# Kernel tuning notes

Measured on AMD Instinct MI355X. Metric: run time of the kernel, lower is better.

The kernel has to match this reference:

```python
import jax, jax.numpy as jnp
import numpy as np

B, V, T, C, HIN, WIN = 1, 6, 3, 256, 32, 32
NH = 8
LN_EPS = 1e-5


def setup_inputs() -> dict:
    key = jax.random.key(0)
    ks = jax.random.split(key, 14)
    s = 0.02
    lim = 1.0 / np.sqrt(C)
    def lin_w(k):
        return jax.random.uniform(k, (C, C), jnp.float32, -lim, lim)
    return {
        "history_feats": jax.random.normal(ks[0], (B, V, T, C, HIN, WIN), jnp.float32),
        "query_embed": jax.random.normal(ks[1], (1, C, 1, 1), jnp.float32) * s,
        "camera_pos_embed": jax.random.normal(ks[2], (V, C), jnp.float32) * s,
        "temporal_pos_embed": jax.random.normal(ks[3], (T, C), jnp.float32) * s,
        "spatial_pos_embed": jax.random.normal(ks[4], (1, C, 1, 1), jnp.float32) * s,
        "q_w": lin_w(ks[5]), "q_b": jnp.zeros((C,), jnp.float32),
        "k_w": lin_w(ks[6]), "k_b": jnp.zeros((C,), jnp.float32),
        "v_w": lin_w(ks[7]), "v_b": jnp.zeros((C,), jnp.float32),
        "o_w": lin_w(ks[8]), "o_b": jnp.zeros((C,), jnp.float32),
        "ln_g": jnp.ones((C,), jnp.float32),
        "ln_b": jnp.zeros((C,), jnp.float32),
        "query_cam_idx": 0,
        "H": 32,
        "W": 32,
    }


def reference(history_feats, query_embed, camera_pos_embed, temporal_pos_embed,
              spatial_pos_embed, q_w, q_b, k_w, k_b, v_w, v_b, o_w, o_b,
              ln_g, ln_b, query_cam_idx, H, W):
    B_, V_, T_, C_, Hin, Win = history_feats.shape
    dh = C_ // NH
    # --- build query: [B, H*W, C] ---
    q = query_embed + camera_pos_embed[query_cam_idx][None, :, None, None] + spatial_pos_embed
    q = jnp.broadcast_to(q, (B_, C_, H, W)).reshape(B_, C_, H * W).transpose(0, 2, 1)
    kv = (history_feats
          + temporal_pos_embed[None, None, :, :, None, None]
          + camera_pos_embed[None, :, None, :, None, None])
    kv = kv.transpose(0, 1, 2, 4, 5, 3).reshape(B_, V_ * T_ * Hin * Win, C_)
    # --- projections (torch Linear: x @ W.T + b) ---
    qp = q @ q_w.T + q_b
    kp = kv @ k_w.T + k_b
    vp = kv @ v_w.T + v_b
    # --- split heads: [B, NH, L, dh] ---
    qh = qp.reshape(B_, H * W, NH, dh).transpose(0, 2, 1, 3)
    kh = kp.reshape(B_, -1, NH, dh).transpose(0, 2, 1, 3)
    vh = vp.reshape(B_, -1, NH, dh).transpose(0, 2, 1, 3)
    scale = float(dh) ** -0.5
    attn = jax.nn.softmax(jnp.einsum('bhqd,bhkd->bhqk', qh, kh) * scale, axis=-1)
    out = jnp.einsum('bhqk,bhkd->bhqd', attn, vh)
    out = out.transpose(0, 2, 1, 3).reshape(B_, H * W, C_)
    out = out @ o_w.T + o_b
    # --- LayerNorm over channel dim ---
    mu = out.mean(-1, keepdims=True)
    var = ((out - mu) ** 2).mean(-1, keepdims=True)
    out = (out - mu) * jax.lax.rsqrt(var + LN_EPS) * ln_g + ln_b
    return out.transpose(0, 2, 1).reshape(B_, C_, H, W)
```

## Files before the change

kernel.cpp:

```cpp
#include <hip/hip_runtime.h>
#include <hip/hip_fp16.h>

typedef const float* fcp;

#define C_    256
#define NH_   8
#define DH_   32
#define VT_   18
#define HWK   1024
#define L_    (VT_*HWK)
#define SCALE_ 0.17677669529663687f

#define EMB_OFF  0
#define WF_OFF   4608
#define BB_OFF   6656
#define PS_OFF   6720
#define Y_OFF    9024
#define Z_OFF    9280
#define CTXP_OFF 9536

__device__ __forceinline__ float blockReduceSum256(float v){
  __shared__ float red[4];
  #pragma unroll
  for (int off = 32; off; off >>= 1) v += __shfl_xor(v, off, 64);
  const int lane = threadIdx.x & 63, w = threadIdx.x >> 6;
  __syncthreads();
  if (lane == 0) red[w] = v;
  __syncthreads();
  return red[0] + red[1] + red[2] + red[3];
}

__global__ void k_fold(fcp qe, fcp cam, fcp tpe, fcp spe, const int* __restrict__ cidx,
                       fcp qw, fcp qb, fcp kw, fcp kb, float* __restrict__ ws){
  __shared__ float qvS[C_];
  __shared__ float qpS[DH_];
  const int b = blockIdx.x, t = threadIdx.x, lane = t & 63, wv = t >> 6;
  const int ci = cidx[0];
  qvS[t] = qe[t] + cam[ci*C_ + t] + spe[t];
  {
    const int v = b/3, tt = b - v*3;
    ws[EMB_OFF + b*C_ + t] = tpe[tt*C_ + t] + cam[v*C_ + t];
  }
  __syncthreads();
  if (b < 8){
    #pragma unroll
    for (int i = 0; i < 8; i++){
      const int r = b*DH_ + wv*8 + i;
      fcp qr = qw + (size_t)r*C_;
      float v = qr[lane]*qvS[lane] + qr[64+lane]*qvS[64+lane]
              + qr[128+lane]*qvS[128+lane] + qr[192+lane]*qvS[192+lane];
      #pragma unroll
      for (int off = 32; off; off >>= 1) v += __shfl_xor(v, off, 64);
      if (lane == 0) qpS[wv*8 + i] = v + qb[r];
    }
    __syncthreads();
    float acc = 0.f;
    #pragma unroll 8
    for (int d = 0; d < DH_; d++)
      acc += qpS[d] * kw[(size_t)(b*DH_ + d)*C_ + t];
    ws[WF_OFF + b*C_ + t] = SCALE_ * acc;
    if (t == 0){
      float bb = 0.f;
      for (int d = 0; d < DH_; d++) bb += qpS[d] * kb[b*DH_ + d];
      ws[BB_OFF + b] = SCALE_ * bb;
    }
  }
}

__global__ void k_attn(fcp feats, float* __restrict__ ws){
  __shared__ __align__(16) float wf[C_*8];
  __shared__ float redS[32];
  __shared__ float basef[8];
  __shared__ __align__(16) float pred[8*512];
  __shared__ float pexS[64*8];
  __shared__ __half fS[8*32*66];
  const int bid = blockIdx.x, vt = bid >> 4, sc = bid & 15, t = threadIdx.x;

  for (int idx = t; idx < 2048; idx += 512){
    const int h = idx >> 8, c = idx & 255;
    wf[c*8 + h] = ws[WF_OFF + idx];
  }
  __syncthreads();
  if (t < 256){
    const float e = ws[EMB_OFF + vt*C_ + t];
    const float4 wa = *(const float4*)&wf[t*8];
    const float4 wb = *(const float4*)&wf[t*8 + 4];
    float pb[8] = {e*wa.x, e*wa.y, e*wa.z, e*wa.w, e*wb.x, e*wb.y, e*wb.z, e*wb.w};
    #pragma unroll
    for (int h = 0; h < 8; h++){
      float v = pb[h];
      #pragma unroll
      for (int off = 32; off; off >>= 1) v += __shfl_xor(v, off, 64);
      if ((t & 63) == 0) redS[(t >> 6)*8 + h] = v;
    }
  }
  __syncthreads();
  if (t < 8) basef[t] = redS[t] + redS[8+t] + redS[16+t] + redS[24+t] + ws[BB_OFF + t];
  __syncthreads();
  const int s = t & 63, cg = t >> 6;
  fcp fp = feats + ((size_t)vt*C_ + cg*32)*HWK + sc*64 + s;
  float acc[8] = {0,0,0,0,0,0,0,0};
  #pragma unroll 8
  for (int i = 0; i < 32; i++){
    const float fv = fp[(size_t)i*HWK];
    fS[(cg*32 + i)*66 + s] = __float2half(fv);
    const float4 wa = *(const float4*)&wf[(cg*32+i)*8];
    const float4 wb = *(const float4*)&wf[(cg*32+i)*8 + 4];
    acc[0] += fv*wa.x; acc[1] += fv*wa.y; acc[2] += fv*wa.z; acc[3] += fv*wa.w;
    acc[4] += fv*wb.x; acc[5] += fv*wb.y; acc[6] += fv*wb.z; acc[7] += fv*wb.w;
  }
  #pragma unroll
  for (int h = 0; h < 8; h++) pred[cg*512 + h*64 + s] = acc[h];
  __syncthreads();
  {
    const int h1 = t >> 6, tok = t & 63;
    float sum = basef[h1];
    #pragma unroll
    for (int cg2 = 0; cg2 < 8; cg2++) sum += pred[cg2*512 + t];
    const float e = __expf(sum);
    pexS[tok*8 + h1] = e;
    float v = e;
    #pragma unroll
    for (int off = 32; off; off >>= 1) v += __shfl_xor(v, off, 64);
    if (tok == 0) ws[PS_OFF + bid*8 + h1] = v;
  }
  __syncthreads();
  const int lane = t & 63, hB = lane & 7, isub = lane >> 3;
  float aB[4] = {0.f, 0.f, 0.f, 0.f};
  #pragma unroll 8
  for (int s2 = 0; s2 < 64; s2++){
    const float pe = pexS[s2*8 + hB];
    #pragma unroll
    for (int p = 0; p < 4; p++)
      aB[p] += pe * __half2float(fS[(cg*32 + p*8 + isub)*66 + s2]);
  }
  float* outp = ws + CTXP_OFF + (size_t)bid*2048;
  #pragma unroll
  for (int p = 0; p < 4; p++)
    outp[hB*256 + cg*32 + p*8 + isub] = aB[p];
}

__global__ void k_vproj(fcp vw, fcp vb, float* __restrict__ ws){
  __shared__ float psS[288*8];
  const int r = blockIdx.x, t = threadIdx.x, h = r >> 5;
  for (int i = t; i < 288*8; i += 256) psS[i] = ws[PS_OFF + i];
  __syncthreads();
  float ctx = 0.f;
  const float* pp = ws + CTXP_OFF + h*256 + t;
  #pragma unroll 8
  for (int b = 0; b < 288; b++) ctx += pp[(size_t)b*2048];
  float denom = 0.f, embP = 0.f;
  for (int vt = 0; vt < VT_; vt++){
    float P = 0.f;
    #pragma unroll
    for (int sc2 = 0; sc2 < 16; sc2++) P += psS[(vt*16 + sc2)*8 + h];
    denom += P;
    embP  += ws[EMB_OFF + vt*C_ + t] * P;
  }
  const float ctxn = (ctx + embP) / denom;
  float v = vw[(size_t)r*C_ + t] * ctxn;
  v = blockReduceSum256(v);
  if (t == 0) ws[Y_OFF + r] = v + vb[r];
}

__global__ void k_oproj(fcp ow, fcp ob, float* __restrict__ ws){
  const int r = blockIdx.x, t = threadIdx.x;
  float v = ow[(size_t)r*C_ + t] * ws[Y_OFF + t];
  v = blockReduceSum256(v);
  if (t == 0) ws[Z_OFF + r] = v + ob[r];
}

__global__ void k_out(fcp lng, fcp lnb, const float* __restrict__ ws,
                      float* __restrict__ out, int hw){
  const int c = blockIdx.x, t = threadIdx.x;
  const float z = ws[Z_OFF + t];
  const float s  = blockReduceSum256(z);
  const float s2 = blockReduceSum256(z*z);
  const float mu = s * (1.f/C_);
  const float var = s2 * (1.f/C_) - mu*mu;
  const float rs = rsqrtf(var + 1e-5f);
  const float fin = (ws[Z_OFF + c] - mu) * rs * lng[c] + lnb[c];
  float4 pk = make_float4(fin, fin, fin, fin);
  ((float4*)(out + (size_t)c*hw))[t] = pk;
}

extern "C" void kernel_launch(void* const* d_in, const int* in_sizes, int n_in,
                              void* d_out, int out_size, void* d_ws, size_t ws_size,
                              hipStream_t stream) {
  fcp feats = (fcp)d_in[0];
  fcp qe    = (fcp)d_in[1];
  fcp cam   = (fcp)d_in[2];
  fcp tpe   = (fcp)d_in[3];
  fcp spe   = (fcp)d_in[4];
  fcp qw    = (fcp)d_in[5];
  fcp qb    = (fcp)d_in[6];
  fcp kw    = (fcp)d_in[7];
  fcp kb    = (fcp)d_in[8];
  fcp vw    = (fcp)d_in[9];
  fcp vb    = (fcp)d_in[10];
  fcp ow    = (fcp)d_in[11];
  fcp ob    = (fcp)d_in[12];
  fcp lng   = (fcp)d_in[13];
  fcp lnb   = (fcp)d_in[14];
  const int* cidx = (const int*)d_in[15];
  float* ws = (float*)d_ws;
  float* out = (float*)d_out;
  const int hw = out_size / C_;

  k_fold  <<<18,  256, 0, stream>>>(qe, cam, tpe, spe, cidx, qw, qb, kw, kb, ws);
  k_attn  <<<288, 512, 0, stream>>>(feats, ws);
  k_vproj <<<256, 256, 0, stream>>>(vw, vb, ws);
  k_oproj <<<256, 256, 0, stream>>>(ow, ob, ws);
  k_out   <<<256, 256, 0, stream>>>(lng, lnb, ws, out, hw);
}
```

Measured before the change: 149.0 us.

## Fuse V/O projection and LayerNorm tail into one kernel with atomic partial sums

Attention blocks now accumulate their per-block softmax denominators and context partials straight into global buffers with atomicAdd, instead of writing 288 partial slices to reduce later. The three tail kernels (V projection, O projection, LayerNorm/broadcast) are merged into one kernel. Each of its 128 blocks redundantly recomputes the whole 256-wide GEMV chain and then writes its slice of the output. The P·V inner loop also reads half2 pairs to halve the shared-memory loads. This removes two kernel launches and the large partial-buffer reduction, at the cost of atomic contention, non-deterministic summation order, and redundant per-block weight reads.

```diff
diff --git a/kernel.cpp b/kernel.cpp
--- a/kernel.cpp
+++ b/kernel.cpp
@@ -14,21 +14,8 @@
 #define EMB_OFF  0
 #define WF_OFF   4608
 #define BB_OFF   6656
-#define PS_OFF   6720
-#define Y_OFF    9024
-#define Z_OFF    9280
-#define CTXP_OFF 9536
-
-__device__ __forceinline__ float blockReduceSum256(float v){
-  __shared__ float red[4];
-  #pragma unroll
-  for (int off = 32; off; off >>= 1) v += __shfl_xor(v, off, 64);
-  const int lane = threadIdx.x & 63, w = threadIdx.x >> 6;
-  __syncthreads();
-  if (lane == 0) red[w] = v;
-  __syncthreads();
-  return red[0] + red[1] + red[2] + red[3];
-}
+#define PSVT_OFF 6720
+#define CTX_OFF  6912
 
 __global__ void k_fold(fcp qe, fcp cam, fcp tpe, fcp spe, const int* __restrict__ cidx,
                        fcp qw, fcp qb, fcp kw, fcp kb, float* __restrict__ ws){
@@ -40,6 +27,11 @@
   {
     const int v = b/3, tt = b - v*3;
     ws[EMB_OFF + b*C_ + t] = tpe[tt*C_ + t] + cam[v*C_ + t];
+  }
+  if (b == 8){
+    #pragma unroll
+    for (int i = 0; i < 8; i++) ws[CTX_OFF + i*256 + t] = 0.f;
+    if (t < 144) ws[PSVT_OFF + t] = 0.f;
   }
   __syncthreads();
   if (b < 8){
@@ -73,7 +65,7 @@
   __shared__ float basef[8];
   __shared__ __align__(16) float pred[8*512];
   __shared__ float pexS[64*8];
-  __shared__ __half fS[8*32*66];
+  __shared__ __align__(16) __half fS[8*32*66];
   const int bid = blockIdx.x, vt = bid >> 4, sc = bid & 15, t = threadIdx.x;
 
   for (int idx = t; idx < 2048; idx += 512){
@@ -122,66 +114,102 @@
     float v = e;
     #pragma unroll
     for (int off = 32; off; off >>= 1) v += __shfl_xor(v, off, 64);
-    if (tok == 0) ws[PS_OFF + bid*8 + h1] = v;
+    if (tok == 0) atomicAdd(&ws[PSVT_OFF + vt*8 + h1], v);
   }
   __syncthreads();
   const int lane = t & 63, hB = lane & 7, isub = lane >> 3;
   float aB[4] = {0.f, 0.f, 0.f, 0.f};
-  #pragma unroll 8
-  for (int s2 = 0; s2 < 64; s2++){
-    const float pe = pexS[s2*8 + hB];
-    #pragma unroll
-    for (int p = 0; p < 4; p++)
-      aB[p] += pe * __half2float(fS[(cg*32 + p*8 + isub)*66 + s2]);
-  }
-  float* outp = ws + CTXP_OFF + (size_t)bid*2048;
+  #pragma unroll 4
+  for (int s2 = 0; s2 < 64; s2 += 2){
+    const float pe0 = pexS[s2*8 + hB];
+    const float pe1 = pexS[s2*8 + 8 + hB];
+    #pragma unroll
+    for (int p = 0; p < 4; p++){
+      const __half2 h2 = *(const __half2*)&fS[(cg*32 + p*8 + isub)*66 + s2];
+      const float2 f2 = __half22float2(h2);
+      aB[p] += pe0 * f2.x + pe1 * f2.y;
+    }
+  }
   #pragma unroll
   for (int p = 0; p < 4; p++)
-    outp[hB*256 + cg*32 + p*8 + isub] = aB[p];
-}
-
-__global__ void k_vproj(fcp vw, fcp vb, float* __restrict__ ws){
-  __shared__ float psS[288*8];
-  const int r = blockIdx.x, t = threadIdx.x, h = r >> 5;
-  for (int i = t; i < 288*8; i += 256) psS[i] = ws[PS_OFF + i];
-  __syncthreads();
-  float ctx = 0.f;
-  const float* pp = ws + CTXP_OFF + h*256 + t;
-  #pragma unroll 8
-  for (int b = 0; b < 288; b++) ctx += pp[(size_t)b*2048];
-  float denom = 0.f, embP = 0.f;
-  for (int vt = 0; vt < VT_; vt++){
-    float P = 0.f;
-    #pragma unroll
-    for (int sc2 = 0; sc2 < 16; sc2++) P += psS[(vt*16 + sc2)*8 + h];
-    denom += P;
-    embP  += ws[EMB_OFF + vt*C_ + t] * P;
-  }
-  const float ctxn = (ctx + embP) / denom;
-  float v = vw[(size_t)r*C_ + t] * ctxn;
-  v = blockReduceSum256(v);
-  if (t == 0) ws[Y_OFF + r] = v + vb[r];
-}
-
-__global__ void k_oproj(fcp ow, fcp ob, float* __restrict__ ws){
-  const int r = blockIdx.x, t = threadIdx.x;
-  float v = ow[(size_t)r*C_ + t] * ws[Y_OFF + t];
-  v = blockReduceSum256(v);
-  if (t == 0) ws[Z_OFF + r] = v + ob[r];
-}
-
-__global__ void k_out(fcp lng, fcp lnb, const float* __restrict__ ws,
-                      float* __restrict__ out, int hw){
-  const int c = blockIdx.x, t = threadIdx.x;
-  const float z = ws[Z_OFF + t];
-  const float s  = blockReduceSum256(z);
-  const float s2 = blockReduceSum256(z*z);
-  const float mu = s * (1.f/C_);
-  const float var = s2 * (1.f/C_) - mu*mu;
-  const float rs = rsqrtf(var + 1e-5f);
-  const float fin = (ws[Z_OFF + c] - mu) * rs * lng[c] + lnb[c];
-  float4 pk = make_float4(fin, fin, fin, fin);
-  ((float4*)(out + (size_t)c*hw))[t] = pk;
+    atomicAdd(&ws[CTX_OFF + hB*256 + cg*32 + p*8 + isub], aB[p]);
+}
+
+__global__ void k_tail(fcp vw, fcp vb, fcp ow, fcp ob, fcp lng, fcp lnb,
+                       fcp wsr, float* __restrict__ out, int hw){
+  __shared__ float PS[144];
+  __shared__ float rdS[8];
+  __shared__ __align__(16) float ctxnS[2048];
+  __shared__ __align__(16) float yS[256];
+  __shared__ float zS[256];
+  __shared__ float redA[8], redB[8], mv[2];
+  const int t = threadIdx.x, w = t >> 6, lane = t & 63;
+  if (t < 144) PS[t] = wsr[PSVT_OFF + t];
+  __syncthreads();
+  if (t < 8){
+    float d = 0.f;
+    #pragma unroll
+    for (int vt = 0; vt < VT_; vt++) d += PS[vt*8 + t];
+    rdS[t] = 1.f / d;
+  }
+  __syncthreads();
+  #pragma unroll
+  for (int hc = t; hc < 2048; hc += 512){
+    const int h = hc >> 8, c = hc & 255;
+    float corr = 0.f;
+    #pragma unroll
+    for (int vt = 0; vt < VT_; vt++) corr += wsr[EMB_OFF + vt*C_ + c] * PS[vt*8 + h];
+    ctxnS[hc] = (wsr[CTX_OFF + hc] + corr) * rdS[h];
+  }
+  __syncthreads();
+  {
+    const float4 cv = *(const float4*)&ctxnS[w*256 + lane*4];
+    #pragma unroll 8
+    for (int i = 0; i < 32; i++){
+      const int k = w*32 + i;
+      const float4 a = *(const float4*)&vw[(size_t)k*C_ + lane*4];
+      float v = a.x*cv.x + a.y*cv.y + a.z*cv.z + a.w*cv.w;
+      #pragma unroll
+      for (int off = 32; off; off >>= 1) v += __shfl_xor(v, off, 64);
+      if (lane == 0) yS[k] = v + vb[k];
+    }
+  }
+  __syncthreads();
+  {
+    const float4 yv = *(const float4*)&yS[lane*4];
+    #pragma unroll 8
+    for (int i = 0; i < 32; i++){
+      const int r = w*32 + i;
+      const float4 a = *(const float4*)&ow[(size_t)r*C_ + lane*4];
+      float v = a.x*yv.x + a.y*yv.y + a.z*yv.z + a.w*yv.w;
+      #pragma unroll
+      for (int off = 32; off; off >>= 1) v += __shfl_xor(v, off, 64);
+      if (lane == 0) zS[r] = v + ob[r];
+    }
+  }
+  __syncthreads();
+  const float zv = (t < 256) ? zS[t] : 0.f;
+  float a1 = zv, a2 = zv*zv;
+  #pragma unroll
+  for (int off = 32; off; off >>= 1){
+    a1 += __shfl_xor(a1, off, 64);
+    a2 += __shfl_xor(a2, off, 64);
+  }
+  if (lane == 0){ redA[w] = a1; redB[w] = a2; }
+  __syncthreads();
+  if (t == 0){
+    float s1 = 0.f, s2 = 0.f;
+    #pragma unroll
+    for (int i = 0; i < 8; i++){ s1 += redA[i]; s2 += redB[i]; }
+    const float mu = s1 * (1.f/C_);
+    const float var = s2 * (1.f/C_) - mu*mu;
+    mv[0] = mu; mv[1] = rsqrtf(var + 1e-5f);
+  }
+  __syncthreads();
+  const int tid = blockIdx.x*512 + t;
+  const int c = tid >> 8, quad = tid & 255;
+  const float fin = (zS[c] - mv[0]) * mv[1] * lng[c] + lnb[c];
+  ((float4*)out)[(size_t)c*(hw >> 2) + quad] = make_float4(fin, fin, fin, fin);
 }
 
 extern "C" void kernel_launch(void* const* d_in, const int* in_sizes, int n_in,
@@ -207,9 +235,7 @@
   float* out = (float*)d_out;
   const int hw = out_size / C_;
 
-  k_fold  <<<18,  256, 0, stream>>>(qe, cam, tpe, spe, cidx, qw, qb, kw, kb, ws);
-  k_attn  <<<288, 512, 0, stream>>>(feats, ws);
-  k_vproj <<<256, 256, 0, stream>>>(vw, vb, ws);
-  k_oproj <<<256, 256, 0, stream>>>(ow, ob, ws);
-  k_out   <<<256, 256, 0, stream>>>(lng, lnb, ws, out, hw);
-}
+  k_fold <<<18,  256, 0, stream>>>(qe, cam, tpe, spe, cidx, qw, qb, kw, kb, ws);
+  k_attn <<<288, 512, 0, stream>>>(feats, ws);
+  k_tail <<<128, 512, 0, stream>>>(vw, vb, ow, ob, lng, lnb, ws, out, hw);
+}
```

Result: slower. 168.5 us (+13.1%).

## Accumulate attention partials with atomics instead of per-block buffers

Applied to the files above, without the earlier changes.

Per-block context partials and exp-sum partials are now accumulated directly into small global buffers with atomicAdd, zeroed in k_fold. This removes the 288x2048 partial buffer write and the per-row 288-way reduction that every k_vproj block repeated. The inner PV loop also reads half2 pairs from shared memory to halve LDS instructions. In exchange there is heavy atomic contention: 288 blocks add into the same 2048 floats, and floating-point summation order becomes nondeterministic.

```diff
diff --git a/kernel.cpp b/kernel.cpp
--- a/kernel.cpp
+++ b/kernel.cpp
@@ -14,10 +14,10 @@
 #define EMB_OFF  0
 #define WF_OFF   4608
 #define BB_OFF   6656
-#define PS_OFF   6720
-#define Y_OFF    9024
-#define Z_OFF    9280
-#define CTXP_OFF 9536
+#define PSVT_OFF 6720
+#define CTX_OFF  6912
+#define Y_OFF    8960
+#define Z_OFF    9216
 
 __device__ __forceinline__ float blockReduceSum256(float v){
   __shared__ float red[4];
@@ -41,6 +41,11 @@
     const int v = b/3, tt = b - v*3;
     ws[EMB_OFF + b*C_ + t] = tpe[tt*C_ + t] + cam[v*C_ + t];
   }
+  if (b == 8){
+    #pragma unroll
+    for (int i = 0; i < 8; i++) ws[CTX_OFF + i*256 + t] = 0.f;
+    if (t < 144) ws[PSVT_OFF + t] = 0.f;
+  }
   __syncthreads();
   if (b < 8){
     #pragma unroll
@@ -73,7 +78,7 @@
   __shared__ float basef[8];
   __shared__ __align__(16) float pred[8*512];
   __shared__ float pexS[64*8];
-  __shared__ __half fS[8*32*66];
+  __shared__ __align__(16) __half fS[8*32*66];
   const int bid = blockIdx.x, vt = bid >> 4, sc = bid & 15, t = threadIdx.x;
 
   for (int idx = t; idx < 2048; idx += 512){
@@ -122,41 +127,40 @@
     float v = e;
     #pragma unroll
     for (int off = 32; off; off >>= 1) v += __shfl_xor(v, off, 64);
-    if (tok == 0) ws[PS_OFF + bid*8 + h1] = v;
+    if (tok == 0) atomicAdd(&ws[PSVT_OFF + vt*8 + h1], v);
   }
   __syncthreads();
   const int lane = t & 63, hB = lane & 7, isub = lane >> 3;
   float aB[4] = {0.f, 0.f, 0.f, 0.f};
-  #pragma unroll 8
-  for (int s2 = 0; s2 < 64; s2++){
-    const float pe = pexS[s2*8 + hB];
-    #pragma unroll
-    for (int p = 0; p < 4; p++)
-      aB[p] += pe * __half2float(fS[(cg*32 + p*8 + isub)*66 + s2]);
-  }
-  float* outp = ws + CTXP_OFF + (size_t)bid*2048;
+  #pragma unroll 4
+  for (int s2 = 0; s2 < 64; s2 += 2){
+    const float pe0 = pexS[s2*8 + hB];
+    const float pe1 = pexS[s2*8 + 8 + hB];
+    #pragma unroll
+    for (int p = 0; p < 4; p++){
+      const __half2 h2 = *(const __half2*)&fS[(cg*32 + p*8 + isub)*66 + s2];
+      const float2 f2 = __half22float2(h2);
+      aB[p] += pe0 * f2.x + pe1 * f2.y;
+    }
+  }
   #pragma unroll
   for (int p = 0; p < 4; p++)
-    outp[hB*256 + cg*32 + p*8 + isub] = aB[p];
+    atomicAdd(&ws[CTX_OFF + hB*256 + cg*32 + p*8 + isub], aB[p]);
 }
 
 __global__ void k_vproj(fcp vw, fcp vb, float* __restrict__ ws){
-  __shared__ float psS[288*8];
+  __shared__ float psS[144];
   const int r = blockIdx.x, t = threadIdx.x, h = r >> 5;
-  for (int i = t; i < 288*8; i += 256) psS[i] = ws[PS_OFF + i];
-  __syncthreads();
-  float ctx = 0.f;
-  const float* pp = ws + CTXP_OFF + h*256 + t;
-  #pragma unroll 8
-  for (int b = 0; b < 288; b++) ctx += pp[(size_t)b*2048];
+  if (t < 144) psS[t] = ws[PSVT_OFF + t];
+  __syncthreads();
   float denom = 0.f, embP = 0.f;
+  #pragma unroll
   for (int vt = 0; vt < VT_; vt++){
-    float P = 0.f;
-    #pragma unroll
-    for (int sc2 = 0; sc2 < 16; sc2++) P += psS[(vt*16 + sc2)*8 + h];
+    const float P = psS[vt*8 + h];
     denom += P;
     embP  += ws[EMB_OFF + vt*C_ + t] * P;
   }
+  const float ctx = ws[CTX_OFF + h*256 + t];
   const float ctxn = (ctx + embP) / denom;
   float v = vw[(size_t)r*C_ + t] * ctxn;
   v = blockReduceSum256(v);
```

After: 137.2 us. -7.9%, faster.
